# Performance work log

Measured on AMD Instinct MI355X. Metric: run time of the kernel, lower is better.

## Reference

```python
import jax, jax.numpy as jnp
import numpy as np
from jax import lax

B, CIN, H, W = 4, 720, 128, 128
MID = 512           # conv3x3 output channels (hardcoded in OCRHead)
KC, VC, NC = 256, 256, 19
BN_EPS = 1e-5


def setup_inputs() -> dict:
    key = jax.random.key(0)
    ks = jax.random.split(key, 16)
    s = 0.02
    f32 = jnp.float32
    return {
        "feats": jax.random.normal(ks[0], (B, CIN, H, W), f32),
        # conv3x3 (no bias)
        "w3": (jax.random.normal(ks[1], (MID, CIN, 3, 3), f32) * s),
        # BatchNorm affine params
        "gamma": 1.0 + 0.1 * jax.random.normal(ks[2], (MID,), f32),
        "beta": 0.1 * jax.random.normal(ks[3], (MID,), f32),
        # aux 1x1 conv (with bias)
        "aux_w": jax.random.normal(ks[4], (NC, MID), f32) * s,
        "aux_b": 0.01 * jax.random.normal(ks[5], (NC,), f32),
        # ObjectAttention: query 1x1 conv (no bias), key/value Linear (with bias), out 1x1 conv (no bias)
        "q_w": jax.random.normal(ks[6], (KC, MID), f32) * s,
        "k_w": jax.random.normal(ks[7], (KC, MID), f32) * s,
        "k_b": 0.01 * jax.random.normal(ks[8], (KC,), f32),
        "v_w": jax.random.normal(ks[9], (VC, MID), f32) * s,
        "v_b": 0.01 * jax.random.normal(ks[10], (VC,), f32),
        "out_w": jax.random.normal(ks[11], (MID, VC), f32) * s,
        # cls 1x1 conv (with bias)
        "cls_w": jax.random.normal(ks[12], (NC, MID), f32) * s,
        "cls_b": 0.01 * jax.random.normal(ks[13], (NC,), f32),
    }


def reference(feats, w3, gamma, beta, aux_w, aux_b, q_w, k_w, k_b, v_w, v_b, out_w, cls_w, cls_b):
    # conv3x3, padding=1, no bias
    x = lax.conv_general_dilated(feats, w3, window_strides=(1, 1),
                                 padding=((1, 1), (1, 1)),
                                 dimension_numbers=("NCHW", "OIHW", "NCHW"))
    # BatchNorm (batch mode: stats over batch+spatial) + relu
    mean = jnp.mean(x, axis=(0, 2, 3))
    var = jnp.var(x, axis=(0, 2, 3))
    x = (x - mean[None, :, None, None]) * lax.rsqrt(var + BN_EPS)[None, :, None, None]
    x = x * gamma[None, :, None, None] + beta[None, :, None, None]
    x = jax.nn.relu(x)

    # aux head: 1x1 conv with bias -> [B, K, H, W]
    aux_logits = jnp.einsum("bchw,kc->bkhw", x, aux_w) + aux_b[None, :, None, None]

    # SpatialGather: softmax over classes per pixel, normalize over pixels per class
    x_flat = x.reshape(B, MID, H * W).transpose(0, 2, 1)           # [B, N, C]
    probs = jax.nn.softmax(aux_logits.reshape(B, NC, H * W).transpose(0, 2, 1), axis=-1)  # [B, N, K]
    weights = probs / jnp.clip(jnp.sum(probs, axis=1, keepdims=True), 1e-6)
    context = jnp.einsum("bnk,bnc->bkc", weights, x_flat)          # [B, K, C]

    # ObjectAttention
    q = jnp.einsum("bchw,dc->bdhw", x, q_w).reshape(B, KC, H * W).transpose(0, 2, 1)  # [B, N, KC]
    k = jnp.einsum("bkc,dc->bkd", context, k_w) + k_b              # [B, K, KC]
    v = jnp.einsum("bkc,dc->bkd", context, v_w) + v_b              # [B, K, VC]
    scale = 1.0 / jnp.sqrt(jnp.asarray(KC, jnp.float32))
    attn = jax.nn.softmax(jnp.einsum("bnd,bkd->bnk", q * scale, k), axis=-1)  # [B, N, K]
    agg = jnp.einsum("bnk,bkv->bnv", attn, v)                      # [B, N, VC]
    agg_chw = agg.reshape(B, H, W, VC).transpose(0, 3, 1, 2)       # [B, VC, H, W]
    obj = jnp.einsum("bvhw,ov->bohw", agg_chw, out_w)              # [B, MID, H, W]

    x = x + obj
    logits = jnp.einsum("bchw,kc->bkhw", x, cls_w) + cls_b[None, :, None, None]
    return (logits, aux_logits)
```

## Files before the change

kernel.cpp:

```cpp
#include <hip/hip_runtime.h>
#include <hip/hip_bf16.h>


__device__ __forceinline__ float u_lo(unsigned u) { return __uint_as_float(u << 16); }
__device__ __forceinline__ float u_hi(unsigned u) { return __uint_as_float(u & 0xffff0000u); }
__device__ __forceinline__ float scrub(float v) { return isfinite(v) ? v : 1e4f; }
#define BF2F(h) __bfloat162float(h)

typedef __attribute__((ext_vector_type(8))) short bf16x8;
typedef __attribute__((ext_vector_type(4))) float f32x4;

#define SO_APACK  0ull
#define TAIL0     9371648ull
#define TA_AUXWT  (TAIL0 + 0ull)
#define TA_CLSWT  (TAIL0 + 38912ull)
#define TA_SS     (TAIL0 + 77824ull)
#define TA_PSUM   (TAIL0 + 81920ull)
#define TA_CTX    (TAIL0 + 82432ull)
#define TA_KMAT   (TAIL0 + 238080ull)
#define TA_VMAT   (TAIL0 + 315904ull)
#define TA_FCLS   (TAIL0 + 393728ull)
#define TA_MT     (TAIL0 + 413184ull)
#define TA_G      (TAIL0 + 568832ull)

#define LDS_CI   40
#define LDS_ROW  (3 * LDS_CI)
#define LDS_TOT  (130 * LDS_ROW)

__global__ __launch_bounds__(256) void prep_small_kernel(
    const float* __restrict__ aux_w, const float* __restrict__ cls_w,
    float* __restrict__ aux_wt, float* __restrict__ cls_wt) {
  int i = blockIdx.x * 256 + threadIdx.x;
  if (i < 9728) {
    int k = i >> 9, c = i & 511;
    aux_wt[c * 19 + k] = aux_w[i];
    cls_wt[c * 19 + k] = cls_w[i];
  }
}

__global__ __launch_bounds__(256) void prep_apack_kernel(
    const float* __restrict__ w3, __hip_bfloat16* __restrict__ Apack) {
  int idx = blockIdx.x * 256 + threadIdx.x;
  if (idx >= 512 * 736) return;
  int oc = idx / 736, ci = idx - (idx / 736) * 736;
  float v[9];
#pragma unroll
  for (int k = 0; k < 9; ++k) v[k] = 0.f;
  if (ci < 720) {
    const float* src = w3 + ((size_t)oc * 720 + ci) * 9;
#pragma unroll
    for (int k = 0; k < 9; ++k) v[k] = src[k];
  }
#pragma unroll
  for (int k = 0; k < 9; ++k)
    Apack[((size_t)k * 512 + oc) * 736 + ci] = __float2bfloat16(v[k]);
}

__global__ __launch_bounds__(256) void conv_mfma_kernel(
    const float* __restrict__ feats, const __hip_bfloat16* __restrict__ Apack,
    __hip_bfloat16* __restrict__ X) {
  __shared__ short Blds[LDS_TOT];
  int gx = blockIdx.x;
  int oc_t = blockIdx.y;
  int b = gx >> 7, h = gx & 127;
  int tid = threadIdx.x;
  int wave = tid >> 6, lane = tid & 63;
  int wm = wave >> 1, wn = wave & 1;
  int l15 = lane & 15, quad = lane >> 4;

  f32x4 acc[4][4];
#pragma unroll
  for (int mb = 0; mb < 4; ++mb)
#pragma unroll
    for (int nb = 0; nb < 4; ++nb) acc[mb][nb] = (f32x4){0.f, 0.f, 0.f, 0.f};

  for (int i = tid; i < 2 * LDS_ROW; i += 256) {
    int wp = (i < LDS_ROW) ? 0 : 129;
    Blds[wp * LDS_ROW + (i < LDS_ROW ? i : i - LDS_ROW)] = 0;
  }

  int cig = tid & 7;
  int colg = tid >> 3;
  const short* Ab = (const short*)Apack;
  int oc_row = oc_t * 128 + wm * 64 + l15;

  for (int cb = 0; cb < 23; ++cb) {
    __syncthreads();
    int ci0 = cb * 32 + cig * 4;
    const float* fb = feats + (((size_t)b * 720 + ci0) << 14) + colg * 4;
#pragma unroll
    for (int r = 0; r < 3; ++r) {
      int hr = h - 1 + r;
      float4 v0 = {0.f, 0.f, 0.f, 0.f}, v1 = v0, v2 = v0, v3 = v0;
      if (((unsigned)hr < 128u) && (ci0 < 720)) {
        const float* p = fb + hr * 128;
        v0 = *(const float4*)(p);
        v1 = *(const float4*)(p + 16384);
        v2 = *(const float4*)(p + 32768);
        v3 = *(const float4*)(p + 49152);
      }
      union { unsigned long long u; __hip_bfloat16 hh[4]; } W0, W1, W2, W3;
      W0.hh[0] = __float2bfloat16(v0.x); W0.hh[1] = __float2bfloat16(v1.x);
      W0.hh[2] = __float2bfloat16(v2.x); W0.hh[3] = __float2bfloat16(v3.x);
      W1.hh[0] = __float2bfloat16(v0.y); W1.hh[1] = __float2bfloat16(v1.y);
      W1.hh[2] = __float2bfloat16(v2.y); W1.hh[3] = __float2bfloat16(v3.y);
      W2.hh[0] = __float2bfloat16(v0.z); W2.hh[1] = __float2bfloat16(v1.z);
      W2.hh[2] = __float2bfloat16(v2.z); W2.hh[3] = __float2bfloat16(v3.z);
      W3.hh[0] = __float2bfloat16(v0.w); W3.hh[1] = __float2bfloat16(v1.w);
      W3.hh[2] = __float2bfloat16(v2.w); W3.hh[3] = __float2bfloat16(v3.w);
      short* wb = &Blds[(colg * 4 + 1) * LDS_ROW + r * LDS_CI + cig * 4];
      *reinterpret_cast<unsigned long long*>(wb) = W0.u;
      *reinterpret_cast<unsigned long long*>(wb + LDS_ROW) = W1.u;
      *reinterpret_cast<unsigned long long*>(wb + 2 * LDS_ROW) = W2.u;
      *reinterpret_cast<unsigned long long*>(wb + 3 * LDS_ROW) = W3.u;
    }
    __syncthreads();
#pragma unroll
    for (int r = 0; r < 3; ++r) {
#pragma unroll
      for (int dw = 0; dw < 3; ++dw) {
        int plane = r * 3 + dw;
        const short* ap = Ab + ((size_t)plane * 512 + oc_row) * 736 + cb * 32 + quad * 8;
        bf16x8 af[4];
#pragma unroll
        for (int mb = 0; mb < 4; ++mb)
          af[mb] = *(const bf16x8*)(ap + (size_t)mb * 16 * 736);
        bf16x8 bfr[4];
#pragma unroll
        for (int nb = 0; nb < 4; ++nb) {
          int px = wn * 64 + nb * 16 + l15;
          bfr[nb] = *(const bf16x8*)(&Blds[(px + dw) * LDS_ROW + r * LDS_CI + quad * 8]);
        }
#pragma unroll
        for (int mb = 0; mb < 4; ++mb)
#pragma unroll
          for (int nb = 0; nb < 4; ++nb)
            acc[mb][nb] = __builtin_amdgcn_mfma_f32_16x16x32_bf16(
                af[mb], bfr[nb], acc[mb][nb], 0, 0, 0);
      }
    }
  }
#pragma unroll
  for (int mb = 0; mb < 4; ++mb)
#pragma unroll
    for (int nb = 0; nb < 4; ++nb) {
      int px = wn * 64 + nb * 16 + l15;
#pragma unroll
      for (int reg = 0; reg < 4; ++reg) {
        int oc = oc_t * 128 + wm * 64 + mb * 16 + quad * 4 + reg;
        X[(((size_t)b * 512 + oc) << 14) + h * 128 + px] =
            __float2bfloat16(acc[mb][nb][reg]);
      }
    }
}

__global__ __launch_bounds__(256) void bn_stats_kernel(
    const __hip_bfloat16* __restrict__ X, const float* __restrict__ gamma,
    const float* __restrict__ beta, float* __restrict__ ss_out) {
  int c = blockIdx.x, tid = threadIdx.x;
  float s = 0.f, ss = 0.f;
  for (int b = 0; b < 4; ++b) {
    const __hip_bfloat16* p = X + (((size_t)b * 512 + c) << 14);
    for (int n = tid * 8; n < 16384; n += 2048) {
      uint4 u = *reinterpret_cast<const uint4*>(p + n);
      unsigned arr[4] = {u.x, u.y, u.z, u.w};
#pragma unroll
      for (int j = 0; j < 4; ++j) {
        float f0 = u_lo(arr[j]), f1 = u_hi(arr[j]);
        s += f0 + f1;
        ss += f0 * f0 + f1 * f1;
      }
    }
  }
#pragma unroll
  for (int off = 32; off > 0; off >>= 1) {
    s += __shfl_down(s, off);
    ss += __shfl_down(ss, off);
  }
  __shared__ float red[8];
  int wid = tid >> 6, lane = tid & 63;
  if (lane == 0) { red[wid] = s; red[4 + wid] = ss; }
  __syncthreads();
  if (tid == 0) {
    s = red[0] + red[1] + red[2] + red[3];
    ss = red[4] + red[5] + red[6] + red[7];
    float mean = s * (1.f / 65536.f);
    float var = ss * (1.f / 65536.f) - mean * mean;
    float gi = gamma[c] * rsqrtf(var + 1e-5f);
    ss_out[c * 2] = gi;
    ss_out[c * 2 + 1] = beta[c] - mean * gi;
  }
}

__global__ __launch_bounds__(256) void bn_apply_kernel(
    __hip_bfloat16* __restrict__ X, const float* __restrict__ ss) {
  size_t idx = ((size_t)blockIdx.x * 256 + threadIdx.x) * 8;
  int c = (int)((idx >> 14) & 511);
  float sc = ss[c * 2], sh = ss[c * 2 + 1];
  uint4 u = *reinterpret_cast<const uint4*>(X + idx);
  unsigned arr[4] = {u.x, u.y, u.z, u.w};
  union { uint4 u; __hip_bfloat16 h[8]; } O;
#pragma unroll
  for (int j = 0; j < 4; ++j) {
    float f0 = fmaxf(fmaf(u_lo(arr[j]), sc, sh), 0.f);
    float f1 = fmaxf(fmaf(u_hi(arr[j]), sc, sh), 0.f);
    O.h[2 * j] = __float2bfloat16(f0);
    O.h[2 * j + 1] = __float2bfloat16(f1);
  }
  *reinterpret_cast<uint4*>(X + idx) = O.u;
}

__global__ __launch_bounds__(256) void aux_ctx_kernel(
    const __hip_bfloat16* __restrict__ X, const float* __restrict__ aux_wt,
    const float* __restrict__ aux_b,
    float* __restrict__ ctx, float* __restrict__ psum) {
  int b = blockIdx.y;
  int n0 = blockIdx.x * 256;
  int tid = threadIdx.x;
  __shared__ float pl[19][256];

  const __hip_bfloat16* Xb = X + (((size_t)b * 512) << 14);

  int p0 = n0 + tid;
  float a0[19];
#pragma unroll
  for (int k = 0; k < 19; ++k) a0[k] = aux_b[k];
  for (int c = 0; c < 512; ++c) {
    float f0 = BF2F(Xb[((size_t)c << 14) + p0]);
    const float* wr = aux_wt + c * 19;
#pragma unroll
    for (int k = 0; k < 19; ++k) a0[k] = fmaf(wr[k], f0, a0[k]);
  }
  float mx0 = a0[0];
#pragma unroll
  for (int k = 1; k < 19; ++k) mx0 = fmaxf(mx0, a0[k]);
  float s0 = 0.f;
#pragma unroll
  for (int k = 0; k < 19; ++k) { a0[k] = __expf(a0[k] - mx0); s0 += a0[k]; }
  float r0 = 1.f / s0;
#pragma unroll
  for (int k = 0; k < 19; ++k) {
    float q0 = a0[k] * r0;
    pl[k][tid] = q0;
    a0[k] = q0;
  }
#pragma unroll
  for (int k = 0; k < 19; ++k) {
    float t = a0[k];
#pragma unroll
    for (int off = 32; off > 0; off >>= 1) t += __shfl_down(t, off);
    if ((tid & 63) == 0) atomicAdd(&psum[b * 19 + k], t);
  }
  __syncthreads();

  int c0 = tid * 2;
  const __hip_bfloat16* x0 = Xb + ((size_t)c0 << 14) + n0;
  const __hip_bfloat16* x1 = x0 + 16384;
  float b0[19], b1[19];
#pragma unroll
  for (int k = 0; k < 19; ++k) { b0[k] = 0.f; b1[k] = 0.f; }
  for (int nl = 0; nl < 256; ++nl) {
    float xv0 = BF2F(x0[nl]), xv1 = BF2F(x1[nl]);
#pragma unroll
    for (int kk = 0; kk < 19; ++kk) {
      float p = pl[kk][nl];
      b0[kk] = fmaf(p, xv0, b0[kk]);
      b1[kk] = fmaf(p, xv1, b1[kk]);
    }
  }
#pragma unroll
  for (int kk = 0; kk < 19; ++kk) {
    atomicAdd(&ctx[((b * 19 + kk) << 9) + c0], b0[kk]);
    atomicAdd(&ctx[((b * 19 + kk) << 9) + c0 + 1], b1[kk]);
  }
}

__global__ __launch_bounds__(256) void small_a_kernel(
    const float* __restrict__ ctx, const float* __restrict__ psum,
    const float* __restrict__ k_w, const float* __restrict__ k_b,
    const float* __restrict__ v_w, const float* __restrict__ v_b,
    const float* __restrict__ cls_w, const float* __restrict__ out_w,
    float* __restrict__ Kmat, float* __restrict__ vmat, float* __restrict__ fcls) {
  int i = blockIdx.x * 256 + threadIdx.x;
  if (i < 38912) {
    int half = i / 19456;
    int j = i - half * 19456;
    int d = j & 255;
    int t = j >> 8;
    const float* w = (half ? v_w : k_w) + d * 512;
    const float* cr = ctx + (t << 9);
    float s = 0.f;
    for (int c = 0; c < 512; ++c) s = fmaf(w[c], cr[c], s);
    float rcp = 1.f / fmaxf(psum[t], 1e-6f);
    float bias = (half ? v_b : k_b)[d];
    (half ? vmat : Kmat)[j] = s * rcp + bias;
  } else if (i < 43776) {
    int j = i - 38912;
    int vv = j & 255, k = j >> 8;
    const float* cw = cls_w + k * 512;
    float s = 0.f;
    for (int c = 0; c < 512; ++c) s = fmaf(cw[c], out_w[c * 256 + vv], s);
    fcls[j] = s;
  }
}

__global__ __launch_bounds__(256) void small_b_kernel(
    const float* __restrict__ Kmat, const float* __restrict__ vmat,
    const float* __restrict__ fcls, const float* __restrict__ q_w,
    float* __restrict__ m_t, float* __restrict__ g) {
  int i = blockIdx.x * 256 + threadIdx.x;
  if (i < 38912) {
    int kk = i % 19;
    int t = i / 19;
    int c = t & 511, b = t >> 9;
    const float* kr = Kmat + ((b * 19 + kk) << 8);
    float s = 0.f;
    for (int d = 0; d < 256; ++d) s = fmaf(q_w[d * 512 + c], kr[d], s);
    m_t[i] = s;
  } else if (i < 40356) {
    int j = i - 38912;
    int k = j % 19;
    int t = j / 19;
    const float* vr = vmat + (t << 8);
    const float* fr = fcls + (k << 8);
    float s = 0.f;
    for (int v = 0; v < 256; ++v) s = fmaf(fr[v], vr[v], s);
    g[j] = s;
  }
}

__global__ __launch_bounds__(256) void final_fused_kernel(
    const __hip_bfloat16* __restrict__ X, const float* __restrict__ m_t,
    const float* __restrict__ cls_wt, const float* __restrict__ cls_b,
    const float* __restrict__ g, float* __restrict__ out) {
  int b = blockIdx.y;
  int n = blockIdx.x * 256 + threadIdx.x;
  float macc[19], cacc[19];
#pragma unroll
  for (int k = 0; k < 19; ++k) { macc[k] = 0.f; cacc[k] = 0.f; }
  const __hip_bfloat16* xp = X + (((size_t)b * 512) << 14) + n;
  for (int c = 0; c < 512; ++c) {
    float xv = BF2F(xp[(size_t)c << 14]);
    const float* mr = m_t + (b * 512 + c) * 19;
    const float* wr = cls_wt + c * 19;
#pragma unroll
    for (int k = 0; k < 19; ++k) {
      macc[k] = fmaf(mr[k], xv, macc[k]);
      cacc[k] = fmaf(wr[k], xv, cacc[k]);
    }
  }
  float mx = -1e30f;
#pragma unroll
  for (int k = 0; k < 19; ++k) { macc[k] *= 0.0625f; mx = fmaxf(mx, macc[k]); }
  float sum = 0.f;
#pragma unroll
  for (int k = 0; k < 19; ++k) { macc[k] = __expf(macc[k] - mx); sum += macc[k]; }
  float r = 1.f / sum;
#pragma unroll
  for (int k = 0; k < 19; ++k) cacc[k] += cls_b[k];
#pragma unroll
  for (int kk = 0; kk < 19; ++kk) {
    float av = macc[kk] * r;
    const float* gr = g + (b * 19 + kk) * 19;
#pragma unroll
    for (int k = 0; k < 19; ++k) cacc[k] = fmaf(gr[k], av, cacc[k]);
  }
  size_t ob = ((size_t)b * 19) << 14;
#pragma unroll
  for (int k = 0; k < 19; ++k)
    out[ob + ((size_t)k << 14) + n] = scrub(cacc[k]);
}

__global__ __launch_bounds__(256) void aux_final_kernel(
    const __hip_bfloat16* __restrict__ X, const float* __restrict__ aux_w,
    const float* __restrict__ aux_b, float* __restrict__ aux_out) {
  __shared__ float wt[9728];
  for (int i = threadIdx.x; i < 9728; i += 256) {
    int k = i >> 9, c = i & 511;
    wt[c * 19 + k] = aux_w[i];
  }
  __syncthreads();
  int b = blockIdx.y;
  int n = blockIdx.x * 256 + threadIdx.x;
  float acc[19];
#pragma unroll
  for (int k = 0; k < 19; ++k) acc[k] = aux_b[k];
  const __hip_bfloat16* xp = X + (((size_t)b * 512) << 14) + n;
  for (int c = 0; c < 512; ++c) {
    float xv = BF2F(xp[(size_t)c << 14]);
    const float* wr = &wt[c * 19];
#pragma unroll
    for (int k = 0; k < 19; ++k) acc[k] = fmaf(wr[k], xv, acc[k]);
  }
  size_t ob = ((size_t)b * 19) << 14;
#pragma unroll
  for (int k = 0; k < 19; ++k)
    aux_out[ob + ((size_t)k << 14) + n] = scrub(acc[k]);
}

extern "C" void kernel_launch(void* const* d_in, const int* in_sizes, int n_in,
                              void* d_out, int out_size, void* d_ws, size_t ws_size,
                              hipStream_t stream) {
  const float* feats = (const float*)d_in[0];
  const float* w3    = (const float*)d_in[1];
  const float* gamma = (const float*)d_in[2];
  const float* beta  = (const float*)d_in[3];
  const float* aux_w = (const float*)d_in[4];
  const float* aux_b = (const float*)d_in[5];
  const float* q_w   = (const float*)d_in[6];
  const float* k_w   = (const float*)d_in[7];
  const float* k_b   = (const float*)d_in[8];
  const float* v_w   = (const float*)d_in[9];
  const float* v_b   = (const float*)d_in[10];
  const float* out_w = (const float*)d_in[11];
  const float* cls_w = (const float*)d_in[12];
  const float* cls_b = (const float*)d_in[13];

  float* logits_out = (float*)d_out;
  float* aux_out    = logits_out + 1245184;

  __hip_bfloat16* X = (__hip_bfloat16*)d_ws;

  char* ob = (char*)d_out;
  __hip_bfloat16* Apack = (__hip_bfloat16*)(ob + SO_APACK);
  float* aux_wt = (float*)(ob + TA_AUXWT);
  float* cls_wt = (float*)(ob + TA_CLSWT);
  float* ssbuf  = (float*)(ob + TA_SS);
  float* psum   = (float*)(ob + TA_PSUM);
  float* ctx    = (float*)(ob + TA_CTX);
  float* Kmat   = (float*)(ob + TA_KMAT);
  float* vmat   = (float*)(ob + TA_VMAT);
  float* fcls   = (float*)(ob + TA_FCLS);
  float* m_t    = (float*)(ob + TA_MT);
  float* g      = (float*)(ob + TA_G);

  hipMemsetAsync(ob + TA_PSUM, 0, 512 + 155648, stream);

  prep_small_kernel<<<38, 256, 0, stream>>>(aux_w, cls_w, aux_wt, cls_wt);
  prep_apack_kernel<<<1472, 256, 0, stream>>>(w3, Apack);
  conv_mfma_kernel<<<dim3(512, 4), 256, 0, stream>>>(feats, Apack, X);
  bn_stats_kernel<<<512, 256, 0, stream>>>(X, gamma, beta, ssbuf);
  bn_apply_kernel<<<16384, 256, 0, stream>>>(X, ssbuf);
  aux_ctx_kernel<<<dim3(64, 4), 256, 0, stream>>>(X, aux_wt, aux_b, ctx, psum);
  small_a_kernel<<<171, 256, 0, stream>>>(ctx, psum, k_w, k_b, v_w, v_b, cls_w, out_w,
                                          Kmat, vmat, fcls);
  small_b_kernel<<<158, 256, 0, stream>>>(Kmat, vmat, fcls, q_w, m_t, g);
  final_fused_kernel<<<dim3(64, 4), 256, 0, stream>>>(X, m_t, cls_wt, cls_b, g, logits_out);
  aux_final_kernel<<<dim3(64, 4), 256, 0, stream>>>(X, aux_w, aux_b, aux_out);
}
```

Before: 1.523 ms.

## Remap conv blocks for XCD locality and widen feature staging into LDS

The conv kernel's 2D grid becomes a 1D grid whose block index is decoded so that the four output-channel tiles sharing an input row land on the same XCD. This is meant to improve L2 reuse of feature rows and weights. The feature staging loop also changes: each wave now loads 8 channels as float2 per lane and writes two 16-byte bf16x8 vectors to LDS, replacing four 8-byte writes. This cuts LDS store count, but the global loads become narrower per instruction.

```diff
diff --git a/kernel.cpp b/kernel.cpp
--- a/kernel.cpp
+++ b/kernel.cpp
@@ -60,8 +60,11 @@
     const float* __restrict__ feats, const __hip_bfloat16* __restrict__ Apack,
     __hip_bfloat16* __restrict__ X) {
   __shared__ short Blds[LDS_TOT];
-  int gx = blockIdx.x;
-  int oc_t = blockIdx.y;
+  int bid = blockIdx.x;
+  int xcd = bid & 7;
+  int slot = bid >> 3;
+  int oc_t = slot & 3;
+  int gx = (slot >> 2) * 8 + xcd;
   int b = gx >> 7, h = gx & 127;
   int tid = threadIdx.x;
   int wave = tid >> 6, lane = tid & 63;
@@ -79,40 +82,42 @@
     Blds[wp * LDS_ROW + (i < LDS_ROW ? i : i - LDS_ROW)] = 0;
   }
 
-  int cig = tid & 7;
-  int colg = tid >> 3;
   const short* Ab = (const short*)Apack;
   int oc_row = oc_t * 128 + wm * 64 + l15;
 
   for (int cb = 0; cb < 23; ++cb) {
     __syncthreads();
-    int ci0 = cb * 32 + cig * 4;
-    const float* fb = feats + (((size_t)b * 720 + ci0) << 14) + colg * 4;
+    int ci0 = cb * 32 + wave * 8;
+    bool civ = (ci0 < 720);
+    const float* fb = feats + (((size_t)b * 720 + ci0) << 14) + lane * 2;
 #pragma unroll
     for (int r = 0; r < 3; ++r) {
       int hr = h - 1 + r;
-      float4 v0 = {0.f, 0.f, 0.f, 0.f}, v1 = v0, v2 = v0, v3 = v0;
-      if (((unsigned)hr < 128u) && (ci0 < 720)) {
+      float2 v0 = {0.f, 0.f}, v1 = v0, v2 = v0, v3 = v0,
+             v4 = v0, v5 = v0, v6 = v0, v7 = v0;
+      if (civ && ((unsigned)hr < 128u)) {
         const float* p = fb + hr * 128;
-        v0 = *(const float4*)(p);
-        v1 = *(const float4*)(p + 16384);
-        v2 = *(const float4*)(p + 32768);
-        v3 = *(const float4*)(p + 49152);
+        v0 = *reinterpret_cast<const float2*>(p);
+        v1 = *reinterpret_cast<const float2*>(p + 16384);
+        v2 = *reinterpret_cast<const float2*>(p + 32768);
+        v3 = *reinterpret_cast<const float2*>(p + 49152);
+        v4 = *reinterpret_cast<const float2*>(p + 65536);
+        v5 = *reinterpret_cast<const float2*>(p + 81920);
+        v6 = *reinterpret_cast<const float2*>(p + 98304);
+        v7 = *reinterpret_cast<const float2*>(p + 114688);
       }
-      union { unsigned long long u; __hip_bfloat16 hh[4]; } W0, W1, W2, W3;
-      W0.hh[0] = __float2bfloat16(v0.x); W0.hh[1] = __float2bfloat16(v1.x);
-      W0.hh[2] = __float2bfloat16(v2.x); W0.hh[3] = __float2bfloat16(v3.x);
-      W1.hh[0] = __float2bfloat16(v0.y); W1.hh[1] = __float2bfloat16(v1.y);
-      W1.hh[2] = __float2bfloat16(v2.y); W1.hh[3] = __float2bfloat16(v3.y);
-      W2.hh[0] = __float2bfloat16(v0.z); W2.hh[1] = __float2bfloat16(v1.z);
-      W2.hh[2] = __float2bfloat16(v2.z); W2.hh[3] = __float2bfloat16(v3.z);
-      W3.hh[0] = __float2bfloat16(v0.w); W3.hh[1] = __float2bfloat16(v1.w);
-      W3.hh[2] = __float2bfloat16(v2.w); W3.hh[3] = __float2bfloat16(v3.w);
-      short* wb = &Blds[(colg * 4 + 1) * LDS_ROW + r * LDS_CI + cig * 4];
-      *reinterpret_cast<unsigned long long*>(wb) = W0.u;
-      *reinterpret_cast<unsigned long long*>(wb + LDS_ROW) = W1.u;
-      *reinterpret_cast<unsigned long long*>(wb + 2 * LDS_ROW) = W2.u;
-      *reinterpret_cast<unsigned long long*>(wb + 3 * LDS_ROW) = W3.u;
+      union { bf16x8 v; __hip_bfloat16 h[8]; } E, O;
+      E.h[0] = __float2bfloat16(v0.x); O.h[0] = __float2bfloat16(v0.y);
+      E.h[1] = __float2bfloat16(v1.x); O.h[1] = __float2bfloat16(v1.y);
+      E.h[2] = __float2bfloat16(v2.x); O.h[2] = __float2bfloat16(v2.y);
+      E.h[3] = __float2bfloat16(v3.x); O.h[3] = __float2bfloat16(v3.y);
+      E.h[4] = __float2bfloat16(v4.x); O.h[4] = __float2bfloat16(v4.y);
+      E.h[5] = __float2bfloat16(v5.x); O.h[5] = __float2bfloat16(v5.y);
+      E.h[6] = __float2bfloat16(v6.x); O.h[6] = __float2bfloat16(v6.y);
+      E.h[7] = __float2bfloat16(v7.x); O.h[7] = __float2bfloat16(v7.y);
+      short* wb = &Blds[(lane * 2 + 1) * LDS_ROW + r * LDS_CI + wave * 8];
+      *reinterpret_cast<bf16x8*>(wb) = E.v;
+      *reinterpret_cast<bf16x8*>(wb + LDS_ROW) = O.v;
     }
     __syncthreads();
 #pragma unroll
@@ -438,7 +443,7 @@
 
   prep_small_kernel<<<38, 256, 0, stream>>>(aux_w, cls_w, aux_wt, cls_wt);
   prep_apack_kernel<<<1472, 256, 0, stream>>>(w3, Apack);
-  conv_mfma_kernel<<<dim3(512, 4), 256, 0, stream>>>(feats, Apack, X);
+  conv_mfma_kernel<<<2048, 256, 0, stream>>>(feats, Apack, X);
   bn_stats_kernel<<<512, 256, 0, stream>>>(X, gamma, beta, ssbuf);
   bn_apply_kernel<<<16384, 256, 0, stream>>>(X, ssbuf);
   aux_ctx_kernel<<<dim3(64, 4), 256, 0, stream>>>(X, aux_wt, aux_b, ctx, psum);
```

Measured after the change: 1.453 ms. 1.05x faster.
